# Optimization experiments

Hardware: AMD Instinct MI355X
Metric: run time of the kernel (lower is better)

The kernel has to match this reference:

```python
import jax, jax.numpy as jnp
import numpy as np

N_NODES = 50000
N_EDGES = 400000
F_IN = 70
E_DIM = 4
HID = 128
HEADS = 4


def _add_self_loops(src, dst, edge_attr, n):
    # PyG GATConv(add_self_loops=True, fill_value='mean' when edge_dim is set):
    # self-loop edge_attr = per-dst-node mean of incoming edge_attr.
    cnt = jax.ops.segment_sum(jnp.ones((src.shape[0],), edge_attr.dtype), dst, n)
    loop_attr = jax.ops.segment_sum(edge_attr, dst, n) / jnp.clip(cnt, 1.0)[:, None]
    loop = jnp.arange(n, dtype=src.dtype)
    return (jnp.concatenate([src, loop]), jnp.concatenate([dst, loop]),
            jnp.concatenate([edge_attr, loop_attr], axis=0))


def _gat_layer(x, src, dst, e_attr, W, a_src, a_dst, We, a_edge, b, concat):
    # W: [in, H*D]; a_src/a_dst/a_edge: [H, D]; We: [edge_dim, H*D]
    n = x.shape[0]
    H, D = a_src.shape
    xs = (x @ W).reshape(n, H, D)                      # [N,H,D]
    s_src = jnp.einsum('nhd,hd->nh', xs, a_src)        # [N,H]
    s_dst = jnp.einsum('nhd,hd->nh', xs, a_dst)
    ee = (e_attr @ We).reshape(-1, H, D)               # [E,H,D]
    s_edge = jnp.einsum('ehd,hd->eh', ee, a_edge)
    alpha = jax.nn.leaky_relu(s_src[src] + s_dst[dst] + s_edge, 0.2)  # [E,H]
    # segment softmax over edges grouped by destination node
    m = jax.ops.segment_max(alpha, dst, n)
    m = jnp.where(jnp.isfinite(m), m, 0.0)
    ex = jnp.exp(alpha - m[dst])
    denom = jax.ops.segment_sum(ex, dst, n)
    alpha = ex / (denom[dst] + 1e-16)
    msg = xs[src] * alpha[..., None]                   # [E,H,D] -- dominant traffic
    agg = jax.ops.segment_sum(msg, dst, n)             # [N,H,D]
    out = agg.reshape(n, H * D) if concat else agg.mean(axis=1)
    return out + b


def _layer_norm(x, g, b, eps=1e-5):
    mu = x.mean(-1, keepdims=True)
    var = ((x - mu) ** 2).mean(-1, keepdims=True)
    return (x - mu) * jax.lax.rsqrt(var + eps) * g + b


def setup_inputs() -> dict:
    key = jax.random.key(0)
    ks = jax.random.split(key, 24)
    f32 = jnp.float32
    node_features = jax.random.normal(ks[0], (N_NODES, F_IN), f32)
    edge_index = jax.random.randint(ks[1], (2, N_EDGES), 0, N_NODES, jnp.int32)
    edge_attr = jax.random.uniform(ks[2], (N_EDGES, E_DIM), f32)
    s = 0.1
    return {
        'node_features': node_features,
        'edge_index': edge_index,
        'edge_attr': edge_attr,
        'W1': jax.random.normal(ks[3], (F_IN, HEADS * HID), f32) * s,
        'as1': jax.random.normal(ks[4], (HEADS, HID), f32) * s,
        'ad1': jax.random.normal(ks[5], (HEADS, HID), f32) * s,
        'We1': jax.random.normal(ks[6], (E_DIM, HEADS * HID), f32) * s,
        'ae1': jax.random.normal(ks[7], (HEADS, HID), f32) * s,
        'b1': jnp.zeros((HEADS * HID,), f32),
        # GAT layer 2: 512 -> 128, 1 head, mean
        'W2': jax.random.normal(ks[8], (HEADS * HID, HID), f32) * s,
        'as2': jax.random.normal(ks[9], (1, HID), f32) * s,
        'ad2': jax.random.normal(ks[10], (1, HID), f32) * s,
        'We2': jax.random.normal(ks[11], (E_DIM, HID), f32) * s,
        'ae2': jax.random.normal(ks[12], (1, HID), f32) * s,
        'b2': jnp.zeros((HID,), f32),
        'ln_g': jnp.ones((HID,), f32),
        'ln_b': jnp.zeros((HID,), f32),
        'pw': jax.random.normal(ks[13], (HID, 8), f32) * s,
        'pb': jnp.zeros((8,), f32),
        'dw': jax.random.normal(ks[14], (HID, 4), f32) * s,
        'db': jnp.zeros((4,), f32),
    }


def reference(node_features, edge_index, edge_attr, W1, as1, ad1, We1, ae1, b1,
              W2, as2, ad2, We2, ae2, b2, ln_g, ln_b, pw, pb, dw, db):
    n = node_features.shape[0]
    src, dst, ea = _add_self_loops(edge_index[0], edge_index[1], edge_attr, n)
    x = jax.nn.gelu(_gat_layer(node_features, src, dst, ea, W1, as1, ad1, We1, ae1, b1, True), approximate=False)
    x = jax.nn.gelu(_gat_layer(x, src, dst, ea, W2, as2, ad2, We2, ae2, b2, False), approximate=False)
    x = _layer_norm(x, ln_g, ln_b)
    return (x @ pw + pb, x @ dw + db)
```

## Files before the change

kernel.cpp:

```cpp
#include <hip/hip_runtime.h>
#include <hip/hip_bf16.h>
#include <math.h>

#define NN 50000
#define NE 400000
#define FIN 70
#define EDIM 4
#define HIDD 128
#define NHEAD 4
constexpr int ET = NE + NN;
constexpr int KP1 = 96;
constexpr int NFP = 72;
constexpr int SCB = (NN + 255) / 256;

constexpr size_t al4(size_t x){ return (x + 3) & ~size_t(3); }
constexpr size_t CNT_O   = 0;
constexpr size_t ZEND    = al4(CNT_O + NN);
constexpr size_t CSR_O   = ZEND;
constexpr size_t BSUM_O  = al4(CSR_O + NN + 1);
constexpr size_t BOFF_O  = al4(BSUM_O + 256);
constexpr size_t EPK_O   = al4(BOFF_O + 256);
constexpr size_t EXF1_O  = al4(EPK_O + (size_t)ET*4);
constexpr size_t EXF2_O  = al4(EXF1_O + (size_t)ET*4);
constexpr size_t SS1_O   = al4(EXF2_O + ET);
constexpr size_t SD1_O   = al4(SS1_O + (size_t)NN*4);
constexpr size_t SS2_O   = al4(SD1_O + (size_t)NN*4);
constexpr size_t SD2_O   = al4(SS2_O + NN);
constexpr size_t CST_O   = al4(SD2_O + NN);
constexpr size_t W1T_O   = al4(CST_O + 2048);
constexpr size_t W2T_O   = al4(W1T_O + 4*128*KP1/2);
constexpr size_t NFB_O   = al4(W2T_O + 128*512/2);
constexpr size_t AGG_O   = al4(NFB_O + (size_t)NN*NFP/2);
constexpr size_t XS2_O   = al4(AGG_O + (size_t)4*NN*KP1/2);

constexpr int VS1 = 0;
constexpr int VD1 = 320;
constexpr int VE1 = 640;
constexpr int VE2 = 656;
constexpr int VS2 = 704;
constexpr int VD2 = 1216;

typedef short s8v __attribute__((ext_vector_type(8)));
typedef float f4v __attribute__((ext_vector_type(4)));

__device__ __forceinline__ unsigned short f2b(float v){
  __hip_bfloat16 b = __float2bfloat16(v);
  return *(unsigned short*)&b;
}
__device__ __forceinline__ float b2f(unsigned u_lo16){
  return __uint_as_float(u_lo16 << 16);
}
__device__ __forceinline__ unsigned pk2(float lo, float hi){
  return (unsigned)f2b(lo) | ((unsigned)f2b(hi) << 16);
}
__device__ __forceinline__ float lrelu(float x){ return x > 0.f ? x : 0.2f * x; }

__device__ __forceinline__ float gelu_fast(float x){
  float z = x * 0.70710678118654752440f;
  float a = fabsf(z);
  float t = 1.f / (1.f + 0.3275911f * a);
  float p = ((((1.061405429f*t - 1.453152027f)*t + 1.421413741f)*t
              - 0.284496736f)*t + 0.254829592f)*t;
  float erfv = 1.f - p * __expf(-a * a);
  erfv = copysignf(erfv, z);
  return 0.5f * x * (1.f + erfv);
}

__global__ void k_deg(const int* __restrict__ ei, int* __restrict__ cnt){
  int e = blockIdx.x * 256 + threadIdx.x;
  if (e >= NE) return;
  atomicAdd(&cnt[ei[NE + e]], 1);
}

__global__ void k_scan1(const int* __restrict__ cnt, int* __restrict__ bsum){
  __shared__ int ws[4];
  int t = threadIdx.x, lane = t & 63, w = t >> 6;
  int i = blockIdx.x * 256 + t;
  int v = (i < NN) ? cnt[i] + 1 : 0;
  for (int o = 32; o; o >>= 1) v += __shfl_down(v, o);
  if (lane == 0) ws[w] = v;
  __syncthreads();
  if (t == 0) bsum[blockIdx.x] = ws[0] + ws[1] + ws[2] + ws[3];
}

__global__ void k_scan2(const int* __restrict__ bsum, int* __restrict__ boff){
  __shared__ int ws[4];
  int t = threadIdx.x, lane = t & 63, w = t >> 6;
  int v = (t < SCB) ? bsum[t] : 0;
  int x = v;
  #pragma unroll
  for (int o = 1; o < 64; o <<= 1){ int u = __shfl_up(x, o); if (lane >= o) x += u; }
  if (lane == 63) ws[w] = x;
  __syncthreads();
  if (w == 0 && lane < 4){
    int y = ws[lane];
    #pragma unroll
    for (int o = 1; o < 4; o <<= 1){ int u = __shfl_up(y, o); if (lane >= o) y += u; }
    ws[lane] = y;
  }
  __syncthreads();
  int incl = x + (w > 0 ? ws[w - 1] : 0);
  if (t < SCB) boff[t] = incl - v;
}

__global__ void k_scan3(const int* __restrict__ cnt, const int* __restrict__ boff,
                        int* __restrict__ csr){
  __shared__ int ws[4];
  int t = threadIdx.x, lane = t & 63, w = t >> 6;
  int i = blockIdx.x * 256 + t;
  int v = (i < NN) ? cnt[i] + 1 : 0;
  int x = v;
  #pragma unroll
  for (int o = 1; o < 64; o <<= 1){ int u = __shfl_up(x, o); if (lane >= o) x += u; }
  if (lane == 63) ws[w] = x;
  __syncthreads();
  if (w == 0 && lane < 4){
    int y = ws[lane];
    #pragma unroll
    for (int o = 1; o < 4; o <<= 1){ int u = __shfl_up(y, o); if (lane >= o) y += u; }
    ws[lane] = y;
  }
  __syncthreads();
  if (i < NN) csr[i + 1] = boff[blockIdx.x] + (w > 0 ? ws[w - 1] : 0) + x;
  if (i == 0) csr[0] = 0;
}

__global__ void k_fill(const int* __restrict__ ei, const float* __restrict__ ea,
                       const int* __restrict__ csr, int* __restrict__ cnt,
                       int4* __restrict__ epk, const float* __restrict__ ss1,
                       const float* __restrict__ sd1, const float* __restrict__ C,
                       float4* __restrict__ exf){
  int e = blockIdx.x * 256 + threadIdx.x;
  if (e >= NE) return;
  int s = ei[e], d = ei[NE + e];
  int r = atomicSub(&cnt[d], 1);
  int p = csr[d] + r - 1;
  float4 a = *(const float4*)&ea[(size_t)e * 4];
  epk[p] = make_int4(s, d, (int)pk2(a.x, a.y), (int)pk2(a.z, a.w));
  float4 ssv = *(const float4*)&ss1[(size_t)s * 4];
  float4 sdv = *(const float4*)&sd1[(size_t)d * 4];
  float e0 = __expf(lrelu(ssv.x + sdv.x + a.x*C[VE1+0] + a.y*C[VE1+4] + a.z*C[VE1+8]  + a.w*C[VE1+12]));
  float e1 = __expf(lrelu(ssv.y + sdv.y + a.x*C[VE1+1] + a.y*C[VE1+5] + a.z*C[VE1+9]  + a.w*C[VE1+13]));
  float e2 = __expf(lrelu(ssv.z + sdv.z + a.x*C[VE1+2] + a.y*C[VE1+6] + a.z*C[VE1+10] + a.w*C[VE1+14]));
  float e3 = __expf(lrelu(ssv.w + sdv.w + a.x*C[VE1+3] + a.y*C[VE1+7] + a.z*C[VE1+11] + a.w*C[VE1+15]));
  exf[p] = make_float4(e0, e1, e2, e3);
}

__global__ void k_loopself(const int* __restrict__ csr, int4* __restrict__ epk,
                           const float* __restrict__ ss1, const float* __restrict__ sd1,
                           const float* __restrict__ C, float4* __restrict__ exf){
  int n = blockIdx.x * 256 + threadIdx.x;
  if (n >= NN) return;
  int a = csr[n], b = csr[n + 1];
  int deg = b - a - 1;
  float s0 = 0.f, s1 = 0.f, s2 = 0.f, s3 = 0.f;
  for (int p = a; p < b - 1; ++p){
    int4 v = epk[p];
    s0 += b2f((unsigned)v.z & 0xffffu); s1 += b2f((unsigned)v.z >> 16);
    s2 += b2f((unsigned)v.w & 0xffffu); s3 += b2f((unsigned)v.w >> 16);
  }
  float inv = 1.f / (float)(deg > 1 ? deg : 1);
  float m0 = s0*inv, m1 = s1*inv, m2 = s2*inv, m3 = s3*inv;
  epk[b - 1] = make_int4(n, n, (int)pk2(m0, m1), (int)pk2(m2, m3));
  float4 ssv = *(const float4*)&ss1[(size_t)n * 4];
  float4 sdv = *(const float4*)&sd1[(size_t)n * 4];
  float e0 = __expf(lrelu(ssv.x + sdv.x + m0*C[VE1+0] + m1*C[VE1+4] + m2*C[VE1+8]  + m3*C[VE1+12]));
  float e1 = __expf(lrelu(ssv.y + sdv.y + m0*C[VE1+1] + m1*C[VE1+5] + m2*C[VE1+9]  + m3*C[VE1+13]));
  float e2 = __expf(lrelu(ssv.z + sdv.z + m0*C[VE1+2] + m1*C[VE1+6] + m2*C[VE1+10] + m3*C[VE1+14]));
  float e3 = __expf(lrelu(ssv.w + sdv.w + m0*C[VE1+3] + m1*C[VE1+7] + m2*C[VE1+11] + m3*C[VE1+15]));
  exf[b - 1] = make_float4(e0, e1, e2, e3);
}

__global__ void k_prep(const float* __restrict__ W1, const float* __restrict__ as1,
                       const float* __restrict__ ad1, const float* __restrict__ We1,
                       const float* __restrict__ ae1, const float* __restrict__ W2,
                       const float* __restrict__ as2, const float* __restrict__ ad2,
                       const float* __restrict__ We2, const float* __restrict__ ae2,
                       float* __restrict__ C){
  int t = threadIdx.x;
  if (t < 280){
    int k = t >> 2, h = t & 3;
    float s = 0.f, d = 0.f;
    for (int dd = 0; dd < 128; ++dd){
      float w = W1[k*512 + h*128 + dd];
      s += w * as1[h*128 + dd];
      d += w * ad1[h*128 + dd];
    }
    C[VS1 + t] = s; C[VD1 + t] = d;
  }
  if (t < 16){
    int k = t >> 2, h = t & 3;
    float s = 0.f;
    for (int dd = 0; dd < 128; ++dd) s += We1[k*512 + h*128 + dd] * ae1[h*128 + dd];
    C[VE1 + t] = s;
  }
  if (t < 4){
    float s = 0.f;
    for (int dd = 0; dd < 128; ++dd) s += We2[t*128 + dd] * ae2[dd];
    C[VE2 + t] = s;
  }
  {
    float s = 0.f, d = 0.f;
    for (int dd = 0; dd < 128; ++dd){
      float w = W2[t*128 + dd];
      s += w * as2[dd];
      d += w * ad2[dd];
    }
    C[VS2 + t] = s; C[VD2 + t] = d;
  }
}

__global__ void k_tw(const float* __restrict__ W1, const float* __restrict__ W2,
                     unsigned short* __restrict__ W1p, unsigned short* __restrict__ W2p){
  int i = blockIdx.x * 256 + threadIdx.x;
  if (i < 12*128*32){
    int kk = i & 31, r = (i >> 5) & 127, ph = i >> 12;
    int h = ph / 3, kf = ph - 3*h;
    int kg = kf*32 + kk;
    float v = (kg < FIN) ? W1[kg*512 + h*128 + r] : 0.f;
    W1p[i] = f2b(v);
  } else {
    int j = i - 12*128*32;
    if (j < 16*128*32){
      int kk = j & 31, r = (j >> 5) & 127, p = j >> 12;
      W2p[j] = f2b(W2[(p*32 + kk)*128 + r]);
    }
  }
}

__global__ __launch_bounds__(256) void k_cnfs1(const float* __restrict__ nf,
    const float* __restrict__ C, unsigned short* __restrict__ nfb,
    float* __restrict__ ss1, float* __restrict__ sd1){
  int lane = threadIdx.x & 63, w = threadIdx.x >> 6;
  int n = blockIdx.x * 4 + w;
  if (n >= NN) return;
  int c0 = lane * 2;
  bool act = lane < 35;
  float v0 = 0.f, v1 = 0.f;
  if (act){
    v0 = nf[(size_t)n * FIN + c0];
    v1 = nf[(size_t)n * FIN + c0 + 1];
  }
  if (lane < 36) *(unsigned*)&nfb[(size_t)n * NFP + c0] = act ? pk2(v0, v1) : 0u;
  float sh[4] = {0,0,0,0}, dh[4] = {0,0,0,0};
  if (act){
    float4 cs0 = *(const float4*)&C[VS1 + c0*4];
    float4 cs1 = *(const float4*)&C[VS1 + (c0+1)*4];
    float4 cd0 = *(const float4*)&C[VD1 + c0*4];
    float4 cd1 = *(const float4*)&C[VD1 + (c0+1)*4];
    sh[0] = v0*cs0.x + v1*cs1.x; sh[1] = v0*cs0.y + v1*cs1.y;
    sh[2] = v0*cs0.z + v1*cs1.z; sh[3] = v0*cs0.w + v1*cs1.w;
    dh[0] = v0*cd0.x + v1*cd1.x; dh[1] = v0*cd0.y + v1*cd1.y;
    dh[2] = v0*cd0.z + v1*cd1.z; dh[3] = v0*cd0.w + v1*cd1.w;
  }
  #pragma unroll
  for (int o = 32; o; o >>= 1){
    #pragma unroll
    for (int h = 0; h < 4; ++h){
      sh[h] += __shfl_xor(sh[h], o);
      dh[h] += __shfl_xor(dh[h], o);
    }
  }
  if (lane == 0){
    *(float4*)&ss1[(size_t)n*4] = make_float4(sh[0], sh[1], sh[2], sh[3]);
    *(float4*)&sd1[(size_t)n*4] = make_float4(dh[0], dh[1], dh[2], dh[3]);
  }
}

__global__ void k_al2(const int4* __restrict__ epk, const float* __restrict__ ss2,
                      const float* __restrict__ sd2, const float* __restrict__ C,
                      float* __restrict__ ex2){
  int p = blockIdx.x * 256 + threadIdx.x;
  if (p >= ET) return;
  int4 pk = epk[p];
  int s = pk.x, d = pk.y;
  float ax = b2f((unsigned)pk.z & 0xffffu), ay = b2f((unsigned)pk.z >> 16);
  float az = b2f((unsigned)pk.w & 0xffffu), aw = b2f((unsigned)pk.w >> 16);
  ex2[p] = __expf(lrelu(ss2[s] + sd2[d] +
             ax*C[VE2] + ay*C[VE2+1] + az*C[VE2+2] + aw*C[VE2+3]));
}

__global__ __launch_bounds__(512, 8) void k_gemm12(
    const unsigned short* __restrict__ agg, const unsigned short* __restrict__ W1p,
    const unsigned short* __restrict__ W2p, const float* __restrict__ b1,
    const float* __restrict__ Cv, unsigned short* __restrict__ xs2b,
    float* __restrict__ ss2, float* __restrict__ sd2){
  __shared__ unsigned short xt[32 * 516];
  __shared__ float ssp[32][4], sdp[32][4];
  int tid = threadIdx.x, lane = tid & 63, w = tid >> 6;
  int wm = w & 1, wn = w >> 1;
  int m15 = lane & 15, rq = lane >> 4;
  int r0 = blockIdx.x * 32;
  int lrow = wm * 16 + m15;
  int gr = r0 + lrow; if (gr >= NN) gr = NN - 1;
  float s2a = 0.f, s2d = 0.f;
  constexpr size_t HS = (size_t)NN * KP1;
  const int bfo = (wn * 32 + m15) * 32 + rq * 8;
  const unsigned short* Ab = agg + (size_t)gr * KP1 + rq * 8;

  #pragma unroll
  for (int h = 0; h < 4; ++h){
    f4v acc[2] = {};
    const unsigned short* Ah = Ab + (size_t)h * HS;
    const unsigned short* Bh = W1p + h * 3 * 4096 + bfo;
    #pragma unroll
    for (int kf = 0; kf < 3; ++kf){
      s8v af = *(const s8v*)(Ah + kf * 32);
      #pragma unroll
      for (int ni = 0; ni < 2; ++ni){
        s8v bf = *(const s8v*)(Bh + kf * 4096 + ni * 512);
        acc[ni] = __builtin_amdgcn_mfma_f32_16x16x32_bf16(bf, af, acc[ni], 0, 0, 0);
      }
    }
    #pragma unroll
    for (int ni = 0; ni < 2; ++ni){
      int cb = h * 128 + wn * 32 + ni * 16 + rq * 4;
      float4 bv = *(const float4*)&b1[cb];
      float v0 = gelu_fast(acc[ni][0] + bv.x);
      float v1 = gelu_fast(acc[ni][1] + bv.y);
      float v2 = gelu_fast(acc[ni][2] + bv.z);
      float v3 = gelu_fast(acc[ni][3] + bv.w);
      float4 cs = *(const float4*)&Cv[VS2 + cb];
      float4 cd = *(const float4*)&Cv[VD2 + cb];
      s2a += v0*cs.x + v1*cs.y + v2*cs.z + v3*cs.w;
      s2d += v0*cd.x + v1*cd.y + v2*cd.z + v3*cd.w;
      *(uint2*)&xt[lrow * 516 + cb] = make_uint2(pk2(v0, v1), pk2(v2, v3));
    }
  }
  s2a += __shfl_xor(s2a, 16); s2a += __shfl_xor(s2a, 32);
  s2d += __shfl_xor(s2d, 16); s2d += __shfl_xor(s2d, 32);
  if (rq == 0){ ssp[lrow][wn] = s2a; sdp[lrow][wn] = s2d; }

  __syncthreads();

  if (tid < 32 && r0 + tid < NN){
    ss2[r0 + tid] = (ssp[tid][0] + ssp[tid][1]) + (ssp[tid][2] + ssp[tid][3]);
    sd2[r0 + tid] = (sdp[tid][0] + sdp[tid][1]) + (sdp[tid][2] + sdp[tid][3]);
  }

  f4v acc2[2] = {};
  #pragma unroll
  for (int p = 0; p < 16; ++p){
    s8v af = *(const s8v*)&xt[lrow * 516 + p * 32 + rq * 8];
    #pragma unroll
    for (int ni = 0; ni < 2; ++ni){
      s8v bf = *(const s8v*)(W2p + p * 4096 + bfo + ni * 512);
      acc2[ni] = __builtin_amdgcn_mfma_f32_16x16x32_bf16(bf, af, acc2[ni], 0, 0, 0);
    }
  }
  int grow = r0 + lrow;
  if (grow < NN){
    #pragma unroll
    for (int ni = 0; ni < 2; ++ni){
      int gc = wn * 32 + ni * 16 + rq * 4;
      *(uint2*)&xs2b[(size_t)grow * 128 + gc] =
          make_uint2(pk2(acc2[ni][0], acc2[ni][1]), pk2(acc2[ni][2], acc2[ni][3]));
    }
  }
}

__global__ __launch_bounds__(256) void k_aggnf(const int* __restrict__ csr,
    const int4* __restrict__ epk, const float4* __restrict__ exf,
    const unsigned short* __restrict__ nfb, unsigned short* __restrict__ agg){
  int lane = threadIdx.x & 63, w = threadIdx.x >> 6;
  int n = blockIdx.x * 4 + w;
  if (n >= NN) return;
  int off = __builtin_amdgcn_readfirstlane(csr[n]);
  int end = __builtin_amdgcn_readfirstlane(csr[n + 1]);
  int col = lane * 2;
  bool act = lane < 36;
  float d0=0,d1=0,d2=0,d3=0;
  float a00=0,a01=0,a10=0,a11=0,a20=0,a21=0,a30=0,a31=0;
  int p = off;
  for (; p + 2 <= end; p += 2){
    int s0 = epk[p].x, s1 = epk[p+1].x;
    float4 e0 = exf[p], e1 = exf[p+1];
    unsigned u0 = 0, u1 = 0;
    if (act){
      u0 = *(const unsigned*)&nfb[(size_t)s0 * NFP + col];
      u1 = *(const unsigned*)&nfb[(size_t)s1 * NFP + col];
    }
    d0 += e0.x + e1.x; d1 += e0.y + e1.y; d2 += e0.z + e1.z; d3 += e0.w + e1.w;
    float v00 = b2f(u0 & 0xffffu), v01 = b2f(u0 >> 16);
    float v10 = b2f(u1 & 0xffffu), v11 = b2f(u1 >> 16);
    a00 += e0.x*v00 + e1.x*v10; a01 += e0.x*v01 + e1.x*v11;
    a10 += e0.y*v00 + e1.y*v10; a11 += e0.y*v01 + e1.y*v11;
    a20 += e0.z*v00 + e1.z*v10; a21 += e0.z*v01 + e1.z*v11;
    a30 += e0.w*v00 + e1.w*v10; a31 += e0.w*v01 + e1.w*v11;
  }
  if (p < end){
    int s0 = epk[p].x;
    float4 e0 = exf[p];
    unsigned u0 = 0;
    if (act) u0 = *(const unsigned*)&nfb[(size_t)s0 * NFP + col];
    d0 += e0.x; d1 += e0.y; d2 += e0.z; d3 += e0.w;
    float v00 = b2f(u0 & 0xffffu), v01 = b2f(u0 >> 16);
    a00 += e0.x*v00; a01 += e0.x*v01;
    a10 += e0.y*v00; a11 += e0.y*v01;
    a20 += e0.z*v00; a21 += e0.z*v01;
    a30 += e0.w*v00; a31 += e0.w*v01;
  }
  float i0 = 1.f/(d0+1e-16f), i1 = 1.f/(d1+1e-16f);
  float i2 = 1.f/(d2+1e-16f), i3 = 1.f/(d3+1e-16f);
  constexpr size_t HS = (size_t)NN * KP1;
  size_t base = (size_t)n * KP1 + col;
  if (act){
    *(unsigned*)&agg[base]        = pk2(a00*i0, a01*i0);
    *(unsigned*)&agg[base +   HS] = pk2(a10*i1, a11*i1);
    *(unsigned*)&agg[base + 2*HS] = pk2(a20*i2, a21*i2);
    *(unsigned*)&agg[base + 3*HS] = pk2(a30*i3, a31*i3);
  } else if (lane < 48){
    *(unsigned*)&agg[base]        = 0u;
    *(unsigned*)&agg[base +   HS] = 0u;
    *(unsigned*)&agg[base + 2*HS] = 0u;
    *(unsigned*)&agg[base + 3*HS] = 0u;
  }
}

__global__ __launch_bounds__(256) void k_agg2(
    const int* __restrict__ csr, const int4* __restrict__ epk,
    const float* __restrict__ ex2, const unsigned short* __restrict__ xs2b,
    const float* __restrict__ b2, const float* __restrict__ lng,
    const float* __restrict__ lnb, const float* __restrict__ pw,
    const float* __restrict__ pb, const float* __restrict__ dwm,
    const float* __restrict__ dbv, float* __restrict__ out){
  int lane = threadIdx.x & 63, w = threadIdx.x >> 6;
  int n = blockIdx.x * 4 + w;
  if (n >= NN) return;
  int off = __builtin_amdgcn_readfirstlane(csr[n]);
  int end = __builtin_amdgcn_readfirstlane(csr[n + 1]);
  int c0 = lane * 2;
  float acc0 = 0.f, acc1 = 0.f, den = 0.f;
  int p = off;
  for (; p + 4 <= end; p += 4){
    int s0 = epk[p].x, s1 = epk[p+1].x, s2 = epk[p+2].x, s3 = epk[p+3].x;
    float e0 = ex2[p], e1 = ex2[p+1], e2 = ex2[p+2], e3 = ex2[p+3];
    unsigned u0 = *(const unsigned*)&xs2b[(size_t)s0 * 128 + c0];
    unsigned u1 = *(const unsigned*)&xs2b[(size_t)s1 * 128 + c0];
    unsigned u2 = *(const unsigned*)&xs2b[(size_t)s2 * 128 + c0];
    unsigned u3 = *(const unsigned*)&xs2b[(size_t)s3 * 128 + c0];
    den += (e0 + e1) + (e2 + e3);
    acc0 += e0*b2f(u0 & 0xffffu) + e1*b2f(u1 & 0xffffu)
          + e2*b2f(u2 & 0xffffu) + e3*b2f(u3 & 0xffffu);
    acc1 += e0*b2f(u0 >> 16) + e1*b2f(u1 >> 16)
          + e2*b2f(u2 >> 16) + e3*b2f(u3 >> 16);
  }
  for (; p + 2 <= end; p += 2){
    int s0 = epk[p].x, s1 = epk[p+1].x;
    float e0 = ex2[p], e1 = ex2[p+1];
    unsigned u0 = *(const unsigned*)&xs2b[(size_t)s0 * 128 + c0];
    unsigned u1 = *(const unsigned*)&xs2b[(size_t)s1 * 128 + c0];
    den += e0 + e1;
    acc0 += e0*b2f(u0 & 0xffffu) + e1*b2f(u1 & 0xffffu);
    acc1 += e0*b2f(u0 >> 16) + e1*b2f(u1 >> 16);
  }
  if (p < end){
    int s0 = epk[p].x;
    float e0 = ex2[p];
    unsigned u0 = *(const unsigned*)&xs2b[(size_t)s0 * 128 + c0];
    den += e0;
    acc0 += e0*b2f(u0 & 0xffffu);
    acc1 += e0*b2f(u0 >> 16);
  }
  float invd = 1.f / (den + 1e-16f);
  float g0 = gelu_fast(acc0 * invd + b2[c0]);
  float g1 = gelu_fast(acc1 * invd + b2[c0 + 1]);
  float s = g0 + g1;
  #pragma unroll
  for (int o = 32; o; o >>= 1) s += __shfl_xor(s, o);
  float mu = s * (1.f / 128.f);
  float e0 = g0 - mu, e1 = g1 - mu;
  float q = e0*e0 + e1*e1;
  #pragma unroll
  for (int o = 32; o; o >>= 1) q += __shfl_xor(q, o);
  float rstd = rsqrtf(q * (1.f / 128.f) + 1e-5f);
  float y0 = e0 * rstd * lng[c0] + lnb[c0];
  float y1 = e1 * rstd * lng[c0 + 1] + lnb[c0 + 1];
  float pr[12];
  #pragma unroll
  for (int jj = 0; jj < 8; ++jj) pr[jj] = y0 * pw[c0*8 + jj] + y1 * pw[(c0+1)*8 + jj];
  #pragma unroll
  for (int jj = 0; jj < 4; ++jj) pr[8+jj] = y0 * dwm[c0*4 + jj] + y1 * dwm[(c0+1)*4 + jj];
  #pragma unroll
  for (int o = 32; o; o >>= 1)
    #pragma unroll
    for (int jj = 0; jj < 12; ++jj) pr[jj] += __shfl_xor(pr[jj], o);
  if (lane == 0){
    #pragma unroll
    for (int jj = 0; jj < 8; ++jj) out[(size_t)n*8 + jj] = pr[jj] + pb[jj];
    #pragma unroll
    for (int jj = 0; jj < 4; ++jj) out[(size_t)NN*8 + (size_t)n*4 + jj] = pr[8+jj] + dbv[jj];
  }
}

extern "C" void kernel_launch(void* const* d_in, const int* in_sizes, int n_in,
                              void* d_out, int out_size, void* d_ws, size_t ws_size,
                              hipStream_t stream){
  const float* nf  = (const float*)d_in[0];
  const int*   ei  = (const int*)  d_in[1];
  const float* ea  = (const float*)d_in[2];
  const float* W1  = (const float*)d_in[3];
  const float* as1 = (const float*)d_in[4];
  const float* ad1 = (const float*)d_in[5];
  const float* We1 = (const float*)d_in[6];
  const float* ae1 = (const float*)d_in[7];
  const float* b1  = (const float*)d_in[8];
  const float* W2  = (const float*)d_in[9];
  const float* as2 = (const float*)d_in[10];
  const float* ad2 = (const float*)d_in[11];
  const float* We2 = (const float*)d_in[12];
  const float* ae2 = (const float*)d_in[13];
  const float* b2  = (const float*)d_in[14];
  const float* lng = (const float*)d_in[15];
  const float* lnb = (const float*)d_in[16];
  const float* pw  = (const float*)d_in[17];
  const float* pb  = (const float*)d_in[18];
  const float* dw  = (const float*)d_in[19];
  const float* db  = (const float*)d_in[20];
  float* out = (float*)d_out;

  float* wf = (float*)d_ws;
  int*      cnt  = (int*)     (wf + CNT_O);
  int*      csr  = (int*)     (wf + CSR_O);
  int*      bsum = (int*)     (wf + BSUM_O);
  int*      boff = (int*)     (wf + BOFF_O);
  int4*     epk  = (int4*)    (wf + EPK_O);
  float4*   exf1 = (float4*)  (wf + EXF1_O);
  float*    ex2  =            (wf + EXF2_O);
  float*    ss1  =            (wf + SS1_O);
  float*    sd1  =            (wf + SD1_O);
  float*    ss2  =            (wf + SS2_O);
  float*    sd2  =            (wf + SD2_O);
  float*    Cc   =            (wf + CST_O);
  unsigned short* W1p = (unsigned short*)(wf + W1T_O);
  unsigned short* W2p = (unsigned short*)(wf + W2T_O);
  unsigned short* nfb = (unsigned short*)(wf + NFB_O);
  unsigned short* agg = (unsigned short*)(wf + AGG_O);
  unsigned short* xs2b= (unsigned short*)(wf + XS2_O);

  hipMemsetAsync(cnt, 0, NN * sizeof(int), stream);
  k_prep<<<1, 512, 0, stream>>>(W1, as1, ad1, We1, ae1, W2, as2, ad2, We2, ae2, Cc);
  k_tw<<<(12*128*32 + 16*128*32 + 255) / 256, 256, 0, stream>>>(W1, W2, W1p, W2p);
  k_cnfs1<<<(NN + 3) / 4, 256, 0, stream>>>(nf, Cc, nfb, ss1, sd1);
  k_deg<<<(NE + 255) / 256, 256, 0, stream>>>(ei, cnt);
  k_scan1<<<SCB, 256, 0, stream>>>(cnt, bsum);
  k_scan2<<<1, 256, 0, stream>>>(bsum, boff);
  k_scan3<<<SCB, 256, 0, stream>>>(cnt, boff, csr);
  k_fill<<<(NE + 255) / 256, 256, 0, stream>>>(ei, ea, csr, cnt, epk, ss1, sd1, Cc, exf1);
  k_loopself<<<(NN + 255) / 256, 256, 0, stream>>>(csr, epk, ss1, sd1, Cc, exf1);
  k_aggnf<<<(NN + 3) / 4, 256, 0, stream>>>(csr, epk, exf1, nfb, agg);
  k_gemm12<<<(NN + 31) / 32, 512, 0, stream>>>(agg, W1p, W2p, b1, Cc, xs2b, ss2, sd2);
  k_al2<<<(ET + 255) / 256, 256, 0, stream>>>(epk, ss2, sd2, Cc, ex2);
  k_agg2<<<(NN + 3) / 4, 256, 0, stream>>>(csr, epk, ex2, xs2b,
                                           b2, lng, lnb, pw, pb, dw, db, out);
}
```

Baseline: 369.9 us.

## Fuse layer-2 attention exp into aggregation and halve GEMM block waves

Removes the separate k_al2 kernel and recomputes the per-edge attention exponent inside k_agg2 from ss2, sd2 and the packed edge attributes, dropping one launch and the ex2 write and reread. k_gemm12 now uses 256 threads per block, with each wave covering both 16-row halves so B-fragment loads are shared across two MFMAs. Costs: the agg2 inner loop now does a random ss2 gather plus an exp per edge and is unrolled by 2 instead of 4, and the GEMM uses more registers per wave.

```diff
diff --git a/kernel.cpp b/kernel.cpp
--- a/kernel.cpp
+++ b/kernel.cpp
@@ -267,69 +267,66 @@
   }
 }
 
-__global__ void k_al2(const int4* __restrict__ epk, const float* __restrict__ ss2,
-                      const float* __restrict__ sd2, const float* __restrict__ C,
-                      float* __restrict__ ex2){
-  int p = blockIdx.x * 256 + threadIdx.x;
-  if (p >= ET) return;
-  int4 pk = epk[p];
-  int s = pk.x, d = pk.y;
-  float ax = b2f((unsigned)pk.z & 0xffffu), ay = b2f((unsigned)pk.z >> 16);
-  float az = b2f((unsigned)pk.w & 0xffffu), aw = b2f((unsigned)pk.w >> 16);
-  ex2[p] = __expf(lrelu(ss2[s] + sd2[d] +
-             ax*C[VE2] + ay*C[VE2+1] + az*C[VE2+2] + aw*C[VE2+3]));
-}
-
-__global__ __launch_bounds__(512, 8) void k_gemm12(
+__global__ __launch_bounds__(256, 4) void k_gemm12(
     const unsigned short* __restrict__ agg, const unsigned short* __restrict__ W1p,
     const unsigned short* __restrict__ W2p, const float* __restrict__ b1,
     const float* __restrict__ Cv, unsigned short* __restrict__ xs2b,
     float* __restrict__ ss2, float* __restrict__ sd2){
   __shared__ unsigned short xt[32 * 516];
   __shared__ float ssp[32][4], sdp[32][4];
-  int tid = threadIdx.x, lane = tid & 63, w = tid >> 6;
-  int wm = w & 1, wn = w >> 1;
+  int tid = threadIdx.x, lane = tid & 63, wn = tid >> 6;
   int m15 = lane & 15, rq = lane >> 4;
   int r0 = blockIdx.x * 32;
-  int lrow = wm * 16 + m15;
-  int gr = r0 + lrow; if (gr >= NN) gr = NN - 1;
-  float s2a = 0.f, s2d = 0.f;
+  int gr0 = r0 + m15;      if (gr0 >= NN) gr0 = NN - 1;
+  int gr1 = r0 + 16 + m15; if (gr1 >= NN) gr1 = NN - 1;
+  float s2a0 = 0.f, s2d0 = 0.f, s2a1 = 0.f, s2d1 = 0.f;
   constexpr size_t HS = (size_t)NN * KP1;
   const int bfo = (wn * 32 + m15) * 32 + rq * 8;
-  const unsigned short* Ab = agg + (size_t)gr * KP1 + rq * 8;
+  const unsigned short* A0 = agg + (size_t)gr0 * KP1 + rq * 8;
+  const unsigned short* A1 = agg + (size_t)gr1 * KP1 + rq * 8;
 
   #pragma unroll
   for (int h = 0; h < 4; ++h){
-    f4v acc[2] = {};
-    const unsigned short* Ah = Ab + (size_t)h * HS;
+    f4v acc[2][2] = {};
     const unsigned short* Bh = W1p + h * 3 * 4096 + bfo;
     #pragma unroll
     for (int kf = 0; kf < 3; ++kf){
-      s8v af = *(const s8v*)(Ah + kf * 32);
+      s8v a0 = *(const s8v*)(A0 + (size_t)h * HS + kf * 32);
+      s8v a1 = *(const s8v*)(A1 + (size_t)h * HS + kf * 32);
       #pragma unroll
       for (int ni = 0; ni < 2; ++ni){
         s8v bf = *(const s8v*)(Bh + kf * 4096 + ni * 512);
-        acc[ni] = __builtin_amdgcn_mfma_f32_16x16x32_bf16(bf, af, acc[ni], 0, 0, 0);
+        acc[0][ni] = __builtin_amdgcn_mfma_f32_16x16x32_bf16(bf, a0, acc[0][ni], 0, 0, 0);
+        acc[1][ni] = __builtin_amdgcn_mfma_f32_16x16x32_bf16(bf, a1, acc[1][ni], 0, 0, 0);
       }
     }
     #pragma unroll
-    for (int ni = 0; ni < 2; ++ni){
-      int cb = h * 128 + wn * 32 + ni * 16 + rq * 4;
-      float4 bv = *(const float4*)&b1[cb];
-      float v0 = gelu_fast(acc[ni][0] + bv.x);
-      float v1 = gelu_fast(acc[ni][1] + bv.y);
-      float v2 = gelu_fast(acc[ni][2] + bv.z);
-      float v3 = gelu_fast(acc[ni][3] + bv.w);
-      float4 cs = *(const float4*)&Cv[VS2 + cb];
-      float4 cd = *(const float4*)&Cv[VD2 + cb];
-      s2a += v0*cs.x + v1*cs.y + v2*cs.z + v3*cs.w;
-      s2d += v0*cd.x + v1*cd.y + v2*cd.z + v3*cd.w;
-      *(uint2*)&xt[lrow * 516 + cb] = make_uint2(pk2(v0, v1), pk2(v2, v3));
-    }
-  }
-  s2a += __shfl_xor(s2a, 16); s2a += __shfl_xor(s2a, 32);
-  s2d += __shfl_xor(s2d, 16); s2d += __shfl_xor(s2d, 32);
-  if (rq == 0){ ssp[lrow][wn] = s2a; sdp[lrow][wn] = s2d; }
+    for (int m = 0; m < 2; ++m){
+      #pragma unroll
+      for (int ni = 0; ni < 2; ++ni){
+        int cb = h * 128 + wn * 32 + ni * 16 + rq * 4;
+        float4 bv = *(const float4*)&b1[cb];
+        float v0 = gelu_fast(acc[m][ni][0] + bv.x);
+        float v1 = gelu_fast(acc[m][ni][1] + bv.y);
+        float v2 = gelu_fast(acc[m][ni][2] + bv.z);
+        float v3 = gelu_fast(acc[m][ni][3] + bv.w);
+        float4 cs = *(const float4*)&Cv[VS2 + cb];
+        float4 cd = *(const float4*)&Cv[VD2 + cb];
+        float pa = v0*cs.x + v1*cs.y + v2*cs.z + v3*cs.w;
+        float pd = v0*cd.x + v1*cd.y + v2*cd.z + v3*cd.w;
+        if (m == 0){ s2a0 += pa; s2d0 += pd; } else { s2a1 += pa; s2d1 += pd; }
+        *(uint2*)&xt[(m * 16 + m15) * 516 + cb] = make_uint2(pk2(v0, v1), pk2(v2, v3));
+      }
+    }
+  }
+  s2a0 += __shfl_xor(s2a0, 16); s2a0 += __shfl_xor(s2a0, 32);
+  s2d0 += __shfl_xor(s2d0, 16); s2d0 += __shfl_xor(s2d0, 32);
+  s2a1 += __shfl_xor(s2a1, 16); s2a1 += __shfl_xor(s2a1, 32);
+  s2d1 += __shfl_xor(s2d1, 16); s2d1 += __shfl_xor(s2d1, 32);
+  if (rq == 0){
+    ssp[m15][wn] = s2a0;      sdp[m15][wn] = s2d0;
+    ssp[16 + m15][wn] = s2a1; sdp[16 + m15][wn] = s2d1;
+  }
 
   __syncthreads();
 
@@ -338,23 +335,29 @@
     sd2[r0 + tid] = (sdp[tid][0] + sdp[tid][1]) + (sdp[tid][2] + sdp[tid][3]);
   }
 
-  f4v acc2[2] = {};
+  f4v acc2[2][2] = {};
   #pragma unroll
   for (int p = 0; p < 16; ++p){
-    s8v af = *(const s8v*)&xt[lrow * 516 + p * 32 + rq * 8];
+    s8v x0 = *(const s8v*)&xt[m15 * 516 + p * 32 + rq * 8];
+    s8v x1 = *(const s8v*)&xt[(16 + m15) * 516 + p * 32 + rq * 8];
     #pragma unroll
     for (int ni = 0; ni < 2; ++ni){
       s8v bf = *(const s8v*)(W2p + p * 4096 + bfo + ni * 512);
-      acc2[ni] = __builtin_amdgcn_mfma_f32_16x16x32_bf16(bf, af, acc2[ni], 0, 0, 0);
-    }
-  }
-  int grow = r0 + lrow;
-  if (grow < NN){
-    #pragma unroll
-    for (int ni = 0; ni < 2; ++ni){
-      int gc = wn * 32 + ni * 16 + rq * 4;
-      *(uint2*)&xs2b[(size_t)grow * 128 + gc] =
-          make_uint2(pk2(acc2[ni][0], acc2[ni][1]), pk2(acc2[ni][2], acc2[ni][3]));
+      acc2[0][ni] = __builtin_amdgcn_mfma_f32_16x16x32_bf16(bf, x0, acc2[0][ni], 0, 0, 0);
+      acc2[1][ni] = __builtin_amdgcn_mfma_f32_16x16x32_bf16(bf, x1, acc2[1][ni], 0, 0, 0);
+    }
+  }
+  #pragma unroll
+  for (int m = 0; m < 2; ++m){
+    int grow = r0 + m * 16 + m15;
+    if (grow < NN){
+      #pragma unroll
+      for (int ni = 0; ni < 2; ++ni){
+        int gc = wn * 32 + ni * 16 + rq * 4;
+        *(uint2*)&xs2b[(size_t)grow * 128 + gc] =
+            make_uint2(pk2(acc2[m][ni][0], acc2[m][ni][1]),
+                       pk2(acc2[m][ni][2], acc2[m][ni][3]));
+      }
     }
   }
 }
@@ -419,7 +422,8 @@
 
 __global__ __launch_bounds__(256) void k_agg2(
     const int* __restrict__ csr, const int4* __restrict__ epk,
-    const float* __restrict__ ex2, const unsigned short* __restrict__ xs2b,
+    const float* __restrict__ ss2, const float* __restrict__ sd2,
+    const float* __restrict__ Cv, const unsigned short* __restrict__ xs2b,
     const float* __restrict__ b2, const float* __restrict__ lng,
     const float* __restrict__ lnb, const float* __restrict__ pw,
     const float* __restrict__ pb, const float* __restrict__ dwm,
@@ -429,35 +433,35 @@
   if (n >= NN) return;
   int off = __builtin_amdgcn_readfirstlane(csr[n]);
   int end = __builtin_amdgcn_readfirstlane(csr[n + 1]);
+  float sd2n = sd2[n];
+  float cv0 = Cv[VE2], cv1 = Cv[VE2+1], cv2 = Cv[VE2+2], cv3 = Cv[VE2+3];
   int c0 = lane * 2;
   float acc0 = 0.f, acc1 = 0.f, den = 0.f;
   int p = off;
-  for (; p + 4 <= end; p += 4){
-    int s0 = epk[p].x, s1 = epk[p+1].x, s2 = epk[p+2].x, s3 = epk[p+3].x;
-    float e0 = ex2[p], e1 = ex2[p+1], e2 = ex2[p+2], e3 = ex2[p+3];
+  for (; p + 2 <= end; p += 2){
+    int4 p0 = epk[p], p1 = epk[p+1];
+    int s0 = p0.x, s1 = p1.x;
+    float sv0 = ss2[s0], sv1 = ss2[s1];
     unsigned u0 = *(const unsigned*)&xs2b[(size_t)s0 * 128 + c0];
     unsigned u1 = *(const unsigned*)&xs2b[(size_t)s1 * 128 + c0];
-    unsigned u2 = *(const unsigned*)&xs2b[(size_t)s2 * 128 + c0];
-    unsigned u3 = *(const unsigned*)&xs2b[(size_t)s3 * 128 + c0];
-    den += (e0 + e1) + (e2 + e3);
-    acc0 += e0*b2f(u0 & 0xffffu) + e1*b2f(u1 & 0xffffu)
-          + e2*b2f(u2 & 0xffffu) + e3*b2f(u3 & 0xffffu);
-    acc1 += e0*b2f(u0 >> 16) + e1*b2f(u1 >> 16)
-          + e2*b2f(u2 >> 16) + e3*b2f(u3 >> 16);
-  }
-  for (; p + 2 <= end; p += 2){
-    int s0 = epk[p].x, s1 = epk[p+1].x;
-    float e0 = ex2[p], e1 = ex2[p+1];
-    unsigned u0 = *(const unsigned*)&xs2b[(size_t)s0 * 128 + c0];
-    unsigned u1 = *(const unsigned*)&xs2b[(size_t)s1 * 128 + c0];
+    float e0 = __expf(lrelu(sv0 + sd2n
+             + b2f((unsigned)p0.z & 0xffffu)*cv0 + b2f((unsigned)p0.z >> 16)*cv1
+             + b2f((unsigned)p0.w & 0xffffu)*cv2 + b2f((unsigned)p0.w >> 16)*cv3));
+    float e1 = __expf(lrelu(sv1 + sd2n
+             + b2f((unsigned)p1.z & 0xffffu)*cv0 + b2f((unsigned)p1.z >> 16)*cv1
+             + b2f((unsigned)p1.w & 0xffffu)*cv2 + b2f((unsigned)p1.w >> 16)*cv3));
     den += e0 + e1;
     acc0 += e0*b2f(u0 & 0xffffu) + e1*b2f(u1 & 0xffffu);
     acc1 += e0*b2f(u0 >> 16) + e1*b2f(u1 >> 16);
   }
   if (p < end){
-    int s0 = epk[p].x;
-    float e0 = ex2[p];
+    int4 p0 = epk[p];
+    int s0 = p0.x;
+    float sv0 = ss2[s0];
     unsigned u0 = *(const unsigned*)&xs2b[(size_t)s0 * 128 + c0];
+    float e0 = __expf(lrelu(sv0 + sd2n
+             + b2f((unsigned)p0.z & 0xffffu)*cv0 + b2f((unsigned)p0.z >> 16)*cv1
+             + b2f((unsigned)p0.w & 0xffffu)*cv2 + b2f((unsigned)p0.w >> 16)*cv3));
     den += e0;
     acc0 += e0*b2f(u0 & 0xffffu);
     acc1 += e0*b2f(u0 >> 16);
@@ -526,7 +530,6 @@
   int*      boff = (int*)     (wf + BOFF_O);
   int4*     epk  = (int4*)    (wf + EPK_O);
   float4*   exf1 = (float4*)  (wf + EXF1_O);
-  float*    ex2  =            (wf + EXF2_O);
   float*    ss1  =            (wf + SS1_O);
   float*    sd1  =            (wf + SD1_O);
   float*    ss2  =            (wf + SS2_O);
@@ -549,8 +552,7 @@
   k_fill<<<(NE + 255) / 256, 256, 0, stream>>>(ei, ea, csr, cnt, epk, ss1, sd1, Cc, exf1);
   k_loopself<<<(NN + 255) / 256, 256, 0, stream>>>(csr, epk, ss1, sd1, Cc, exf1);
   k_aggnf<<<(NN + 3) / 4, 256, 0, stream>>>(csr, epk, exf1, nfb, agg);
-  k_gemm12<<<(NN + 31) / 32, 512, 0, stream>>>(agg, W1p, W2p, b1, Cc, xs2b, ss2, sd2);
-  k_al2<<<(ET + 255) / 256, 256, 0, stream>>>(epk, ss2, sd2, Cc, ex2);
-  k_agg2<<<(NN + 3) / 4, 256, 0, stream>>>(csr, epk, ex2, xs2b,
+  k_gemm12<<<(NN + 31) / 32, 256, 0, stream>>>(agg, W1p, W2p, b1, Cc, xs2b, ss2, sd2);
+  k_agg2<<<(NN + 3) / 4, 256, 0, stream>>>(csr, epk, ss2, sd2, Cc, xs2b,
                                            b2, lng, lnb, pw, pb, dw, db, out);
 }
```

Result: faster. 344.9 us (-6.8%).
